# Kernel tuning notes

Hardware: AMD Instinct MI355X
Metric: run time of the kernel (lower is better)

The kernel has to match this reference:

```python
import jax, jax.numpy as jnp
import numpy as np

N_EMBD = 1024
N_HEAD = 16
B, T = 4, 2048
EPS = 1e-5


def setup_inputs() -> dict:
    key = jax.random.key(0)
    ks = jax.random.split(key, 12)
    s = 0.02
    d, dff = N_EMBD, 4 * N_EMBD
    return {
        "x": jax.random.normal(ks[0], (B, T, d), dtype=jnp.float32),
        "ln1_w": jnp.ones((d,), jnp.float32),
        "ln1_b": jnp.zeros((d,), jnp.float32),
        "ln2_w": jnp.ones((d,), jnp.float32),
        "ln2_b": jnp.zeros((d,), jnp.float32),
        "w_attn": jax.random.normal(ks[1], (d, 3 * d), jnp.float32) * s,
        "b_attn": jnp.zeros((3 * d,), jnp.float32),
        "w_proj": jax.random.normal(ks[2], (d, d), jnp.float32) * s,
        "b_proj": jnp.zeros((d,), jnp.float32),
        "w_fc": jax.random.normal(ks[3], (d, dff), jnp.float32) * s,
        "b_fc": jnp.zeros((dff,), jnp.float32),
        "w_fc2": jax.random.normal(ks[4], (dff, d), jnp.float32) * s,
        "b_fc2": jnp.zeros((d,), jnp.float32),
    }


def _layernorm(x, w, b):
    mu = jnp.mean(x, axis=-1, keepdims=True)
    var = jnp.mean(jnp.square(x - mu), axis=-1, keepdims=True)
    return (x - mu) * jax.lax.rsqrt(var + EPS) * w + b


def reference(x, ln1_w, ln1_b, ln2_w, ln2_b, w_attn, b_attn, w_proj, b_proj,
              w_fc, b_fc, w_fc2, b_fc2):
    Bx, Tx, C = x.shape
    hd = C // N_HEAD
    # --- attention branch ---
    h = _layernorm(x, ln1_w, ln1_b)
    qkv = h @ w_attn + b_attn  # [B,T,3C]
    q, k, v = jnp.split(qkv, 3, axis=-1)
    q = q.reshape(Bx, Tx, N_HEAD, hd).transpose(0, 2, 1, 3)  # [B,H,T,hd]
    k = k.reshape(Bx, Tx, N_HEAD, hd).transpose(0, 2, 1, 3)
    v = v.reshape(Bx, Tx, N_HEAD, hd).transpose(0, 2, 1, 3)
    att = jnp.einsum("bhqd,bhkd->bhqk", q, k) * (1.0 / np.sqrt(hd))
    causal = jnp.tril(jnp.ones((Tx, Tx), dtype=bool))
    att = jnp.where(causal[None, None], att, -jnp.inf)
    att = jax.nn.softmax(att, axis=-1)
    y = jnp.einsum("bhqk,bhkd->bhqd", att, v)
    y = y.transpose(0, 2, 1, 3).reshape(Bx, Tx, C)
    x = x + (y @ w_proj + b_proj)
    # --- mlp branch ---
    h2 = _layernorm(x, ln2_w, ln2_b)
    m = jax.nn.gelu(h2 @ w_fc + b_fc, approximate=False)
    x = x + (m @ w_fc2 + b_fc2)
    return x
```

## Files before the change

### kernel.cpp

```cpp
#include <hip/hip_runtime.h>
#include <hip/hip_bf16.h>
#include <math.h>

typedef __bf16 bf16;
typedef __bf16 bf16x4 __attribute__((ext_vector_type(4)));
typedef __bf16 bf16x8 __attribute__((ext_vector_type(8)));
typedef float f32x4 __attribute__((ext_vector_type(4)));

__device__ __forceinline__ void gload_lds16(const bf16* g, bf16* l) {
  __builtin_amdgcn_global_load_lds(
      (const __attribute__((address_space(1))) void*)g,
      (__attribute__((address_space(3))) void*)l, 16, 0, 0);
}

#define MF(a, b, c) __builtin_amdgcn_mfma_f32_16x16x32_bf16((a), (b), (c), 0, 0, 0)
#define VM4_BAR()  asm volatile("s_waitcnt vmcnt(4)\ns_barrier" ::: "memory")
#define VM2_BAR()  asm volatile("s_waitcnt vmcnt(2)\ns_barrier" ::: "memory")
#define VM0_BAR()  asm volatile("s_waitcnt vmcnt(0)\ns_barrier" ::: "memory")
#define LGK0_SB()  do { asm volatile("s_waitcnt lgkmcnt(0)" ::: "memory"); \
                        __builtin_amdgcn_sched_barrier(0); } while (0)

template <int EPI, int KSPLIT>
__global__ __launch_bounds__(512, 2)
void gemmq(const bf16* __restrict__ A, const bf16* __restrict__ BT,
           const float* __restrict__ bias, const float* __restrict__ res,
           void* __restrict__ Cout, void* __restrict__ Cout2,
           int M, int N, int K)
{
  __shared__ alignas(16) bf16 lsA[2][16384];
  __shared__ alignas(16) bf16 lsB[2][16384];

  int nbn = N >> 8;
  int nwg = (M >> 8) * nbn;
  int bid = blockIdx.x;
  int ks = 0;
  if (KSPLIT == 2) { ks = (bid >= nwg) ? 1 : 0; bid -= ks * nwg; }
  int cpx = nwg >> 3;
  int wg  = (bid & 7) * cpx + (bid >> 3);
  int m0 = (wg / nbn) << 8;
  int n0 = (wg % nbn) << 8;

  int t = threadIdx.x;
  int l = t & 63, w = t >> 6;
  int wr = (w >> 2) << 6;
  int wc = (w & 3) << 5;
  int lr = l & 15, lg = l >> 4;

  int kb0 = (KSPLIT == 2) ? ks * (K >> 1) : 0;
  int nt = (K / KSPLIT) >> 6;

  const bf16* Ag = A  + (size_t)m0 * K + kb0;
  const bf16* Bg = BT + (size_t)n0 * K + kb0;

  int swz0 = (lg ^ (lr & 7)) << 3;
  int swz1 = swz0 ^ 32;
  int aRow = (wr + lr) << 6;
  int bRow = (wc + lr) << 6;

  const bf16* srcA[2]; const bf16* srcB[2];
#pragma unroll
  for (int j = 0; j < 2; ++j) {
    int ci = j * 512 + t;
    int r = ci >> 3;
    int g = (ci & 7) ^ (r & 7);
    srcA[j] = Ag + (size_t)r * K + g * 8;
    srcB[j] = Bg + (size_t)r * K + g * 8;
  }
  size_t qA = (size_t)128 * K;

#define STAGE_A(q, kofs, db) do { \
  _Pragma("unroll") \
  for (int j = 0; j < 2; ++j) \
    gload_lds16(srcA[j] + (q) * qA + (kofs), &lsA[db][(q) * 8192 + (j * 512 + t) * 8]); \
} while (0)
#define STAGE_B(q, kofs, db) do { \
  _Pragma("unroll") \
  for (int j = 0; j < 2; ++j) \
    gload_lds16(srcB[j] + (q) * qA + (kofs), &lsB[db][(q) * 8192 + (j * 512 + t) * 8]); \
} while (0)

  f32x4 acc[2][2][4][2];
  f32x4 zero = {0.f, 0.f, 0.f, 0.f};
#pragma unroll
  for (int qa = 0; qa < 2; ++qa)
#pragma unroll
    for (int qb = 0; qb < 2; ++qb)
#pragma unroll
      for (int mi = 0; mi < 4; ++mi)
#pragma unroll
        for (int ni = 0; ni < 2; ++ni) acc[qa][qb][mi][ni] = zero;

  STAGE_A(0, 0, 0);
  STAGE_B(0, 0, 0);
  STAGE_B(1, 0, 0);
  STAGE_A(1, 0, 0);

  bf16x8 afr[4][2], bfr0[2][2], bfr1[2][2];

  for (int T = 0; T < nt; ++T) {
    int c = T & 1, d = c ^ 1;
    bool st = (T + 1 < nt);
    int k64 = (T + 1) << 6;
    const bf16* pa = &lsA[c][0];
    const bf16* pb = &lsB[c][0];

    VM4_BAR();
#pragma unroll
    for (int mi = 0; mi < 4; ++mi) {
      afr[mi][0] = *(const bf16x8*)(pa + aRow + mi * 1024 + swz0);
      afr[mi][1] = *(const bf16x8*)(pa + aRow + mi * 1024 + swz1);
    }
#pragma unroll
    for (int ni = 0; ni < 2; ++ni) {
      bfr0[ni][0] = *(const bf16x8*)(pb + bRow + ni * 1024 + swz0);
      bfr0[ni][1] = *(const bf16x8*)(pb + bRow + ni * 1024 + swz1);
    }
    if (st) STAGE_A(0, k64, d);
    LGK0_SB();
    __builtin_amdgcn_s_setprio(1);
#pragma unroll
    for (int mi = 0; mi < 4; ++mi)
#pragma unroll
      for (int ni = 0; ni < 2; ++ni)
#pragma unroll
        for (int kk = 0; kk < 2; ++kk)
          acc[0][0][mi][ni] = MF(afr[mi][kk], bfr0[ni][kk], acc[0][0][mi][ni]);
    __builtin_amdgcn_s_setprio(0);

    if (st) VM4_BAR(); else VM2_BAR();
#pragma unroll
    for (int ni = 0; ni < 2; ++ni) {
      bfr1[ni][0] = *(const bf16x8*)(pb + 8192 + bRow + ni * 1024 + swz0);
      bfr1[ni][1] = *(const bf16x8*)(pb + 8192 + bRow + ni * 1024 + swz1);
    }
    if (st) STAGE_B(0, k64, d);
    LGK0_SB();
    __builtin_amdgcn_s_setprio(1);
#pragma unroll
    for (int mi = 0; mi < 4; ++mi)
#pragma unroll
      for (int ni = 0; ni < 2; ++ni)
#pragma unroll
        for (int kk = 0; kk < 2; ++kk)
          acc[0][1][mi][ni] = MF(afr[mi][kk], bfr1[ni][kk], acc[0][1][mi][ni]);
    __builtin_amdgcn_s_setprio(0);

    if (st) VM4_BAR(); else VM0_BAR();
#pragma unroll
    for (int mi = 0; mi < 4; ++mi) {
      afr[mi][0] = *(const bf16x8*)(pa + 8192 + aRow + mi * 1024 + swz0);
      afr[mi][1] = *(const bf16x8*)(pa + 8192 + aRow + mi * 1024 + swz1);
    }
    if (st) STAGE_B(1, k64, d);
    LGK0_SB();
    __builtin_amdgcn_s_setprio(1);
#pragma unroll
    for (int mi = 0; mi < 4; ++mi)
#pragma unroll
      for (int ni = 0; ni < 2; ++ni)
#pragma unroll
        for (int kk = 0; kk < 2; ++kk)
          acc[1][1][mi][ni] = MF(afr[mi][kk], bfr1[ni][kk], acc[1][1][mi][ni]);
    __builtin_amdgcn_s_setprio(0);

    if (st) STAGE_A(1, k64, d);
    __builtin_amdgcn_s_setprio(1);
#pragma unroll
    for (int mi = 0; mi < 4; ++mi)
#pragma unroll
      for (int ni = 0; ni < 2; ++ni)
#pragma unroll
        for (int kk = 0; kk < 2; ++kk)
          acc[1][0][mi][ni] = MF(afr[mi][kk], bfr0[ni][kk], acc[1][0][mi][ni]);
    __builtin_amdgcn_s_setprio(0);
  }

  bf16* Pb = (bf16*)((KSPLIT == 2 && ks) ? Cout2 : Cout);
#pragma unroll
  for (int qa = 0; qa < 2; ++qa)
#pragma unroll
    for (int mi = 0; mi < 4; ++mi) {
      int row = m0 + qa * 128 + wr + mi * 16 + lg * 4;
#pragma unroll
      for (int qb = 0; qb < 2; ++qb)
#pragma unroll
        for (int ni = 0; ni < 2; ++ni) {
          int col = n0 + qb * 128 + wc + ni * 16 + lr;
          float bv = (EPI == 3) ? 0.f : bias[col];
          f32x4 a = acc[qa][qb][mi][ni];
#pragma unroll
          for (int r = 0; r < 4; ++r) {
            float v = a[r] + bv;
            size_t idx = (size_t)(row + r) * N + col;
            if (EPI == 0)      Pb[idx] = (bf16)v;
            else if (EPI == 1) ((float*)Cout)[idx] = v + res[idx];
            else if (EPI == 2) Pb[idx] = (bf16)(0.5f * v * (1.f + erff(v * 0.70710678118654752f)));
            else               Pb[idx] = (bf16)v;
          }
        }
    }
#undef STAGE_A
#undef STAGE_B
}

__global__ __launch_bounds__(256)
void combine2(const bf16* __restrict__ p0, const bf16* __restrict__ p1,
              const float* __restrict__ bias, const float* __restrict__ res,
              float* __restrict__ out)
{
  int i = (blockIdx.x * 256 + threadIdx.x) * 8;
  bf16x8 a = *(const bf16x8*)(p0 + i);
  bf16x8 b = *(const bf16x8*)(p1 + i);
  int c = i & 1023;
#pragma unroll
  for (int j = 0; j < 8; ++j)
    out[i + j] = (float)a[j] + (float)b[j] + bias[c + j] + res[i + j];
}

__global__ __launch_bounds__(256)
void combine_ln(const bf16* __restrict__ p0, const bf16* __restrict__ p1,
                const float* __restrict__ bias, const float* __restrict__ res,
                const float* __restrict__ lnw, const float* __restrict__ lnb,
                float* __restrict__ x1, bf16* __restrict__ hout)
{
  int row = blockIdx.x;
  int t = threadIdx.x;
  size_t i0 = (size_t)row * 1024 + t * 4;
  bf16x4 a = *(const bf16x4*)(p0 + i0);
  bf16x4 b = *(const bf16x4*)(p1 + i0);
  float4 r = *(const float4*)(res + i0);
  float4 bi = ((const float4*)bias)[t];
  float v0 = (float)a[0] + (float)b[0] + bi.x + r.x;
  float v1 = (float)a[1] + (float)b[1] + bi.y + r.y;
  float v2 = (float)a[2] + (float)b[2] + bi.z + r.z;
  float v3 = (float)a[3] + (float)b[3] + bi.w + r.w;
  float4 vv = {v0, v1, v2, v3};
  *(float4*)(x1 + i0) = vv;
  float s  = v0 + v1 + v2 + v3;
  float sq = v0 * v0 + v1 * v1 + v2 * v2 + v3 * v3;
#pragma unroll
  for (int off = 32; off >= 1; off >>= 1) {
    s  += __shfl_xor(s, off);
    sq += __shfl_xor(sq, off);
  }
  __shared__ float ps[4], pq[4];
  if ((t & 63) == 0) { ps[t >> 6] = s; pq[t >> 6] = sq; }
  __syncthreads();
  s  = ps[0] + ps[1] + ps[2] + ps[3];
  sq = pq[0] + pq[1] + pq[2] + pq[3];
  float mu  = s * (1.f / 1024.f);
  float var = sq * (1.f / 1024.f) - mu * mu;
  float rstd = rsqrtf(var + 1e-5f);
  float4 wv = ((const float4*)lnw)[t];
  float4 bv = ((const float4*)lnb)[t];
  hout[i0 + 0] = (bf16)((v0 - mu) * rstd * wv.x + bv.x);
  hout[i0 + 1] = (bf16)((v1 - mu) * rstd * wv.y + bv.y);
  hout[i0 + 2] = (bf16)((v2 - mu) * rstd * wv.z + bv.z);
  hout[i0 + 3] = (bf16)((v3 - mu) * rstd * wv.w + bv.w);
}

__global__ __launch_bounds__(256)
void ln_bf16(const float* __restrict__ x, const float* __restrict__ w,
             const float* __restrict__ b, bf16* __restrict__ out)
{
  int row = blockIdx.x;
  int t = threadIdx.x;
  float4 v = ((const float4*)(x + (size_t)row * 1024))[t];
  float s  = v.x + v.y + v.z + v.w;
  float sq = v.x * v.x + v.y * v.y + v.z * v.z + v.w * v.w;
#pragma unroll
  for (int off = 32; off >= 1; off >>= 1) {
    s  += __shfl_xor(s, off);
    sq += __shfl_xor(sq, off);
  }
  __shared__ float ps[4], pq[4];
  if ((t & 63) == 0) { ps[t >> 6] = s; pq[t >> 6] = sq; }
  __syncthreads();
  s  = ps[0] + ps[1] + ps[2] + ps[3];
  sq = pq[0] + pq[1] + pq[2] + pq[3];
  float mu  = s * (1.f / 1024.f);
  float var = sq * (1.f / 1024.f) - mu * mu;
  float rstd = rsqrtf(var + 1e-5f);
  float4 wv = ((const float4*)w)[t];
  float4 bv = ((const float4*)b)[t];
  size_t o0 = (size_t)row * 1024 + t * 4;
  out[o0 + 0] = (bf16)((v.x - mu) * rstd * wv.x + bv.x);
  out[o0 + 1] = (bf16)((v.y - mu) * rstd * wv.y + bv.y);
  out[o0 + 2] = (bf16)((v.z - mu) * rstd * wv.z + bv.z);
  out[o0 + 3] = (bf16)((v.w - mu) * rstd * wv.w + bv.w);
}

__global__ __launch_bounds__(256)
void transpose_cast(const float* __restrict__ W, bf16* __restrict__ WT, int K, int N)
{
  __shared__ float tile[32][33];
  int bk = blockIdx.x * 32, bn = blockIdx.y * 32;
  int tx = threadIdx.x & 31, ty = threadIdx.x >> 5;
#pragma unroll
  for (int i = ty; i < 32; i += 8)
    tile[i][tx] = W[(size_t)(bk + i) * N + bn + tx];
  __syncthreads();
#pragma unroll
  for (int i = ty; i < 32; i += 8)
    WT[(size_t)(bn + i) * K + bk + tx] = (bf16)tile[tx][i];
}

__global__ __launch_bounds__(256)
void vtrans(const bf16* __restrict__ qkv, bf16* __restrict__ vt)
{
  __shared__ alignas(16) bf16 tile[64 * 64];
  int bh = blockIdx.x;
  int b = bh >> 4, h = bh & 15;
  int t0 = blockIdx.y * 64;
  int t = threadIdx.x;
#pragma unroll
  for (int i = 0; i < 2; ++i) {
    int c = i * 256 + t;
    int tt = c >> 3, d8 = c & 7;
    bf16x8 v = *(const bf16x8*)(qkv + (size_t)(b * 2048 + t0 + tt) * 3072 + 2048 + h * 64 + d8 * 8);
    *(bf16x8*)&tile[(tt * 8 + (d8 ^ (tt >> 3))) * 8] = v;
  }
  __syncthreads();
#pragma unroll
  for (int i = 0; i < 2; ++i) {
    int c = i * 256 + t;
    int d = c >> 3, tt8 = c & 7;
    bf16x8 o;
#pragma unroll
    for (int j = 0; j < 8; ++j) {
      int row = tt8 * 8 + j;
      o[j] = tile[(row * 8 + ((d >> 3) ^ (row >> 3))) * 8 + (d & 7)];
    }
    *(bf16x8*)(vt + (size_t)(bh * 64 + d) * 2048 + t0 + tt8 * 8) = o;
  }
}

__global__ __launch_bounds__(256)
void attn_flash(const bf16* __restrict__ qkv, const bf16* __restrict__ vt,
                bf16* __restrict__ y)
{
  __shared__ alignas(16) bf16 lk[2][4096];
  __shared__ alignas(16) bf16 lv[2][4096];
  __shared__ alignas(16) bf16 lp[4][16 * 64];

  int bid = blockIdx.x;
  int bh = bid & 63;
  int qb = 31 - (bid >> 6);
  int b = bh >> 4, h = bh & 15;
  int t = threadIdx.x;
  int w = t >> 6, l = t & 63;
  int lr = l & 15, lg = l >> 4;
  int q0 = qb * 64;
  int qw = q0 + w * 16;
  const size_t RS = 3072;
  const float SCL = 0.18033688011112042f;

  const bf16* qbase = qkv + (size_t)(b * 2048) * RS + h * 64;
  const bf16* kbase = qkv + (size_t)(b * 2048) * RS + 1024 + h * 64;
  const bf16* vtb   = vt + (size_t)(bh * 64) * 2048;

  bf16x8 qf[2];
#pragma unroll
  for (int kk = 0; kk < 2; ++kk)
    qf[kk] = *(const bf16x8*)(qbase + (size_t)(qw + lr) * RS + kk * 32 + lg * 8);

  const bf16* pK[2]; const bf16* pV[2]; int dst[2];
#pragma unroll
  for (int i = 0; i < 2; ++i) {
    int c = i * 256 + t;
    int row = c >> 3, c8 = c & 7;
    int sc8 = c8 ^ (row & 7);
    pK[i] = kbase + (size_t)row * RS + sc8 * 8;
    pV[i] = vtb + (size_t)row * 2048 + sc8 * 8;
    dst[i] = c * 8;
  }

  f32x4 zero = {0.f, 0.f, 0.f, 0.f};
  f32x4 o[4];
#pragma unroll
  for (int ni = 0; ni < 4; ++ni) o[ni] = zero;
  float lo[4] = {0.f, 0.f, 0.f, 0.f};

  int nkb = qb + 1;
#pragma unroll
  for (int i = 0; i < 2; ++i) {
    gload_lds16(pK[i], &lk[0][dst[i]]);
    gload_lds16(pV[i], &lv[0][dst[i]]);
  }

  for (int kb = 0; kb < nkb; ++kb) {
    int cur = kb & 1;
    int k0 = kb * 64;
    VM0_BAR();
    if (kb + 1 < nkb) {
#pragma unroll
      for (int i = 0; i < 2; ++i) {
        pK[i] += 64 * RS;
        pV[i] += 64;
        gload_lds16(pK[i], &lk[cur ^ 1][dst[i]]);
        gload_lds16(pV[i], &lv[cur ^ 1][dst[i]]);
      }
    }

    f32x4 s[4];
#pragma unroll
    for (int j = 0; j < 4; ++j) s[j] = zero;
#pragma unroll
    for (int kk = 0; kk < 2; ++kk)
#pragma unroll
      for (int j = 0; j < 4; ++j) {
        int krow = j * 16 + lr;
        bf16x8 kf = *(const bf16x8*)&lk[cur][krow * 64 + (((4 * kk + lg) ^ (krow & 7)) * 8)];
        s[j] = MF(qf[kk], kf, s[j]);
      }

    bool needmask = (kb == qb);
    float p[4][4];
#pragma unroll
    for (int r = 0; r < 4; ++r) {
      int tq = qw + lg * 4 + r;
#pragma unroll
      for (int j = 0; j < 4; ++j) {
        float v = s[j][r] * SCL;
        if (needmask && (k0 + j * 16 + lr > tq)) v = -1e30f;
        p[j][r] = exp2f(v);
      }
      lo[r] += (p[0][r] + p[1][r]) + (p[2][r] + p[3][r]);
    }

#pragma unroll
    for (int r = 0; r < 4; ++r) {
      int qr = lg * 4 + r;
#pragma unroll
      for (int j = 0; j < 4; ++j) {
        int ch = (2 * j + (lr >> 3)) ^ (qr & 7);
        lp[w][qr * 64 + ch * 8 + (lr & 7)] = (bf16)p[j][r];
      }
    }
    bf16x8 pa[2];
#pragma unroll
    for (int kf = 0; kf < 2; ++kf)
      pa[kf] = *(const bf16x8*)&lp[w][lr * 64 + (((4 * kf + lg) ^ (lr & 7)) * 8)];

#pragma unroll
    for (int ni = 0; ni < 4; ++ni)
#pragma unroll
      for (int kf = 0; kf < 2; ++kf) {
        int d = ni * 16 + lr;
        bf16x8 vf = *(const bf16x8*)&lv[cur][d * 64 + (((4 * kf + lg) ^ (d & 7)) * 8)];
        o[ni] = MF(pa[kf], vf, o[ni]);
      }
  }

#pragma unroll
  for (int r = 0; r < 4; ++r) {
#pragma unroll
    for (int off = 1; off < 16; off <<= 1) lo[r] += __shfl_xor(lo[r], off);
    lo[r] = 1.f / lo[r];
  }
#pragma unroll
  for (int ni = 0; ni < 4; ++ni)
#pragma unroll
    for (int r = 0; r < 4; ++r) {
      int tq = qw + lg * 4 + r;
      y[(size_t)(b * 2048 + tq) * 1024 + h * 64 + ni * 16 + lr] = (bf16)(o[ni][r] * lo[r]);
    }
}

extern "C" void kernel_launch(void* const* d_in, const int* in_sizes, int n_in,
                              void* d_out, int out_size, void* d_ws, size_t ws_size,
                              hipStream_t stream) {
  (void)in_sizes; (void)n_in; (void)out_size; (void)ws_size;
  const float* x      = (const float*)d_in[0];
  const float* ln1w   = (const float*)d_in[1];
  const float* ln1b   = (const float*)d_in[2];
  const float* ln2w   = (const float*)d_in[3];
  const float* ln2b   = (const float*)d_in[4];
  const float* w_attn = (const float*)d_in[5];
  const float* b_attn = (const float*)d_in[6];
  const float* w_proj = (const float*)d_in[7];
  const float* b_proj = (const float*)d_in[8];
  const float* w_fc   = (const float*)d_in[9];
  const float* b_fc   = (const float*)d_in[10];
  const float* w_fc2  = (const float*)d_in[11];
  const float* b_fc2  = (const float*)d_in[12];
  float* out = (float*)d_out;

  char* p = (char*)d_ws;
  bf16*  h     = (bf16*)p;  p += (size_t)8192 * 1024 * 2;
  bf16*  qkv   = (bf16*)p;
  bf16*  mbuf  = (bf16*)p;  p += (size_t)8192 * 3072 * 2;
  bf16*  ybuf  = (bf16*)p;  p += (size_t)8192 * 1024 * 2;
  float* x1    = (float*)p; p += (size_t)8192 * 1024 * 4;
  bf16*  wqkvT = (bf16*)p;  p += (size_t)3072 * 1024 * 2;
  bf16*  wprojT= (bf16*)p;  p += (size_t)1024 * 1024 * 2;
  bf16*  wfcT  = (bf16*)p;  p += (size_t)4096 * 1024 * 2;
  bf16*  wfc2T = (bf16*)p;  p += (size_t)1024 * 4096 * 2;
  bf16*  vt    = (bf16*)x1;
  bf16*  pp0   = qkv;
  bf16*  pp1   = qkv + (size_t)8192 * 1024;
  bf16*  sp0   = h;
  bf16*  sp1   = wqkvT;

  transpose_cast<<<dim3(1024 / 32, 3072 / 32), 256, 0, stream>>>(w_attn, wqkvT, 1024, 3072);
  transpose_cast<<<dim3(1024 / 32, 1024 / 32), 256, 0, stream>>>(w_proj, wprojT, 1024, 1024);
  transpose_cast<<<dim3(1024 / 32, 4096 / 32), 256, 0, stream>>>(w_fc,   wfcT,  1024, 4096);
  transpose_cast<<<dim3(4096 / 32, 1024 / 32), 256, 0, stream>>>(w_fc2,  wfc2T, 4096, 1024);

  ln_bf16<<<8192, 256, 0, stream>>>(x, ln1w, ln1b, h);
  gemmq<0, 1><<<384, 512, 0, stream>>>(h, wqkvT, b_attn, nullptr, qkv, nullptr, 8192, 3072, 1024);
  vtrans<<<dim3(64, 32), 256, 0, stream>>>(qkv, vt);
  attn_flash<<<2048, 256, 0, stream>>>(qkv, vt, ybuf);
  gemmq<3, 2><<<256, 512, 0, stream>>>(ybuf, wprojT, nullptr, nullptr, pp0, pp1, 8192, 1024, 1024);
  combine_ln<<<8192, 256, 0, stream>>>(pp0, pp1, b_proj, x, ln2w, ln2b, x1, h);
  gemmq<2, 1><<<512, 512, 0, stream>>>(h, wfcT, b_fc, nullptr, mbuf, nullptr, 8192, 4096, 1024);
  gemmq<3, 2><<<256, 512, 0, stream>>>(mbuf, wfc2T, nullptr, nullptr, sp0, sp1, 8192, 1024, 4096);
  combine2<<<4096, 256, 0, stream>>>(sp0, sp1, b_fc2, x1, out);
}
```

Measured before the change: 409.5 us.

## Replace interleaved quarter-tile staging with single wait and bulk prefetch per K-step

The GEMM main loop used to interleave four quarter-tile global-to-LDS stages with fine-grained vmcnt waits and barriers between four MFMA groups. It now waits for all loads (vmcnt 0) once per K-step, issues all next-tile stages together, then reads every A/B fragment from LDS and runs all four MFMA groups back to back. This simplifies synchronization and cuts the number of barriers, but it raises register pressure with more live fragments and loses the overlap of load completion with partial compute. Dropping the explicit lgkmcnt wait leaves fragment ordering to the compiler.

```diff
diff --git a/kernel.cpp b/kernel.cpp
--- a/kernel.cpp
+++ b/kernel.cpp
@@ -14,11 +14,7 @@
 }
 
 #define MF(a, b, c) __builtin_amdgcn_mfma_f32_16x16x32_bf16((a), (b), (c), 0, 0, 0)
-#define VM4_BAR()  asm volatile("s_waitcnt vmcnt(4)\ns_barrier" ::: "memory")
-#define VM2_BAR()  asm volatile("s_waitcnt vmcnt(2)\ns_barrier" ::: "memory")
 #define VM0_BAR()  asm volatile("s_waitcnt vmcnt(0)\ns_barrier" ::: "memory")
-#define LGK0_SB()  do { asm volatile("s_waitcnt lgkmcnt(0)" ::: "memory"); \
-                        __builtin_amdgcn_sched_barrier(0); } while (0)
 
 template <int EPI, int KSPLIT>
 __global__ __launch_bounds__(512, 2)
@@ -95,7 +91,7 @@
   STAGE_B(1, 0, 0);
   STAGE_A(1, 0, 0);
 
-  bf16x8 afr[4][2], bfr0[2][2], bfr1[2][2];
+  bf16x8 a0[4][2], a1[4][2], b0[2][2], b1[2][2];
 
   for (int T = 0; T < nt; ++T) {
     int c = T & 1, d = c ^ 1;
@@ -104,19 +100,35 @@
     const bf16* pa = &lsA[c][0];
     const bf16* pb = &lsB[c][0];
 
-    VM4_BAR();
+    VM0_BAR();
+    if (st) {
+      STAGE_A(0, k64, d);
+      STAGE_B(0, k64, d);
+      STAGE_B(1, k64, d);
+      STAGE_A(1, k64, d);
+    }
+
 #pragma unroll
     for (int mi = 0; mi < 4; ++mi) {
-      afr[mi][0] = *(const bf16x8*)(pa + aRow + mi * 1024 + swz0);
-      afr[mi][1] = *(const bf16x8*)(pa + aRow + mi * 1024 + swz1);
+      a0[mi][0] = *(const bf16x8*)(pa + aRow + mi * 1024 + swz0);
+      a0[mi][1] = *(const bf16x8*)(pa + aRow + mi * 1024 + swz1);
     }
 #pragma unroll
     for (int ni = 0; ni < 2; ++ni) {
-      bfr0[ni][0] = *(const bf16x8*)(pb + bRow + ni * 1024 + swz0);
-      bfr0[ni][1] = *(const bf16x8*)(pb + bRow + ni * 1024 + swz1);
-    }
-    if (st) STAGE_A(0, k64, d);
-    LGK0_SB();
+      b0[ni][0] = *(const bf16x8*)(pb + bRow + ni * 1024 + swz0);
+      b0[ni][1] = *(const bf16x8*)(pb + bRow + ni * 1024 + swz1);
+    }
+#pragma unroll
+    for (int ni = 0; ni < 2; ++ni) {
+      b1[ni][0] = *(const bf16x8*)(pb + 8192 + bRow + ni * 1024 + swz0);
+      b1[ni][1] = *(const bf16x8*)(pb + 8192 + bRow + ni * 1024 + swz1);
+    }
+#pragma unroll
+    for (int mi = 0; mi < 4; ++mi) {
+      a1[mi][0] = *(const bf16x8*)(pa + 8192 + aRow + mi * 1024 + swz0);
+      a1[mi][1] = *(const bf16x8*)(pa + 8192 + aRow + mi * 1024 + swz1);
+    }
+
     __builtin_amdgcn_s_setprio(1);
 #pragma unroll
     for (int mi = 0; mi < 4; ++mi)
@@ -124,54 +136,28 @@
       for (int ni = 0; ni < 2; ++ni)
 #pragma unroll
         for (int kk = 0; kk < 2; ++kk)
-          acc[0][0][mi][ni] = MF(afr[mi][kk], bfr0[ni][kk], acc[0][0][mi][ni]);
-    __builtin_amdgcn_s_setprio(0);
-
-    if (st) VM4_BAR(); else VM2_BAR();
-#pragma unroll
-    for (int ni = 0; ni < 2; ++ni) {
-      bfr1[ni][0] = *(const bf16x8*)(pb + 8192 + bRow + ni * 1024 + swz0);
-      bfr1[ni][1] = *(const bf16x8*)(pb + 8192 + bRow + ni * 1024 + swz1);
-    }
-    if (st) STAGE_B(0, k64, d);
-    LGK0_SB();
-    __builtin_amdgcn_s_setprio(1);
+          acc[0][0][mi][ni] = MF(a0[mi][kk], b0[ni][kk], acc[0][0][mi][ni]);
 #pragma unroll
     for (int mi = 0; mi < 4; ++mi)
 #pragma unroll
       for (int ni = 0; ni < 2; ++ni)
 #pragma unroll
         for (int kk = 0; kk < 2; ++kk)
-          acc[0][1][mi][ni] = MF(afr[mi][kk], bfr1[ni][kk], acc[0][1][mi][ni]);
-    __builtin_amdgcn_s_setprio(0);
-
-    if (st) VM4_BAR(); else VM0_BAR();
-#pragma unroll
-    for (int mi = 0; mi < 4; ++mi) {
-      afr[mi][0] = *(const bf16x8*)(pa + 8192 + aRow + mi * 1024 + swz0);
-      afr[mi][1] = *(const bf16x8*)(pa + 8192 + aRow + mi * 1024 + swz1);
-    }
-    if (st) STAGE_B(1, k64, d);
-    LGK0_SB();
-    __builtin_amdgcn_s_setprio(1);
+          acc[0][1][mi][ni] = MF(a0[mi][kk], b1[ni][kk], acc[0][1][mi][ni]);
 #pragma unroll
     for (int mi = 0; mi < 4; ++mi)
 #pragma unroll
       for (int ni = 0; ni < 2; ++ni)
 #pragma unroll
         for (int kk = 0; kk < 2; ++kk)
-          acc[1][1][mi][ni] = MF(afr[mi][kk], bfr1[ni][kk], acc[1][1][mi][ni]);
-    __builtin_amdgcn_s_setprio(0);
-
-    if (st) STAGE_A(1, k64, d);
-    __builtin_amdgcn_s_setprio(1);
+          acc[1][1][mi][ni] = MF(a1[mi][kk], b1[ni][kk], acc[1][1][mi][ni]);
 #pragma unroll
     for (int mi = 0; mi < 4; ++mi)
 #pragma unroll
       for (int ni = 0; ni < 2; ++ni)
 #pragma unroll
         for (int kk = 0; kk < 2; ++kk)
-          acc[1][0][mi][ni] = MF(afr[mi][kk], bfr0[ni][kk], acc[1][0][mi][ni]);
+          acc[1][0][mi][ni] = MF(a1[mi][kk], b0[ni][kk], acc[1][0][mi][ni]);
     __builtin_amdgcn_s_setprio(0);
   }
 
```

After: 422.2 us. 3.1% more time.

## Double attention query tile to 128 rows and fold softmax scale into QKV epilogue

Applied to the files above, without the earlier changes.

The flash attention kernel now runs 8 waves per block over 128 query rows instead of 4 waves over 64. Each K/V tile loaded into LDS is therefore shared by twice as many query rows, which halves global K/V traffic and block count. The causal mask check becomes per-wave, since blocks now span two diagonal key tiles. The softmax scale (with log2e) is moved into the QKV GEMM epilogue for the Q columns, removing a multiply per score. This rounds scaled Q to bf16, which slightly changes numerics, and the larger blocks may reduce occupancy and leave diagonal-tile waves with more masked work.

```diff
diff --git a/kernel.cpp b/kernel.cpp
--- a/kernel.cpp
+++ b/kernel.cpp
@@ -175,6 +175,7 @@
     __builtin_amdgcn_s_setprio(0);
   }
 
+  const float SCLQ = 0.18033688011112042f;
   bf16* Pb = (bf16*)((KSPLIT == 2 && ks) ? Cout2 : Cout);
 #pragma unroll
   for (int qa = 0; qa < 2; ++qa)
@@ -195,6 +196,7 @@
             if (EPI == 0)      Pb[idx] = (bf16)v;
             else if (EPI == 1) ((float*)Cout)[idx] = v + res[idx];
             else if (EPI == 2) Pb[idx] = (bf16)(0.5f * v * (1.f + erff(v * 0.70710678118654752f)));
+            else if (EPI == 4) Pb[idx] = (bf16)((col < 1024) ? v * SCLQ : v);
             else               Pb[idx] = (bf16)v;
           }
         }
@@ -335,25 +337,24 @@
   }
 }
 
-__global__ __launch_bounds__(256)
+__global__ __launch_bounds__(512)
 void attn_flash(const bf16* __restrict__ qkv, const bf16* __restrict__ vt,
                 bf16* __restrict__ y)
 {
   __shared__ alignas(16) bf16 lk[2][4096];
   __shared__ alignas(16) bf16 lv[2][4096];
-  __shared__ alignas(16) bf16 lp[4][16 * 64];
+  __shared__ alignas(16) bf16 lp[8][16 * 64];
 
   int bid = blockIdx.x;
   int bh = bid & 63;
-  int qb = 31 - (bid >> 6);
+  int qb = 15 - (bid >> 6);
   int b = bh >> 4, h = bh & 15;
   int t = threadIdx.x;
   int w = t >> 6, l = t & 63;
   int lr = l & 15, lg = l >> 4;
-  int q0 = qb * 64;
+  int q0 = qb * 128;
   int qw = q0 + w * 16;
   const size_t RS = 3072;
-  const float SCL = 0.18033688011112042f;
 
   const bf16* qbase = qkv + (size_t)(b * 2048) * RS + h * 64;
   const bf16* kbase = qkv + (size_t)(b * 2048) * RS + 1024 + h * 64;
@@ -364,16 +365,11 @@
   for (int kk = 0; kk < 2; ++kk)
     qf[kk] = *(const bf16x8*)(qbase + (size_t)(qw + lr) * RS + kk * 32 + lg * 8);
 
-  const bf16* pK[2]; const bf16* pV[2]; int dst[2];
-#pragma unroll
-  for (int i = 0; i < 2; ++i) {
-    int c = i * 256 + t;
-    int row = c >> 3, c8 = c & 7;
-    int sc8 = c8 ^ (row & 7);
-    pK[i] = kbase + (size_t)row * RS + sc8 * 8;
-    pV[i] = vtb + (size_t)row * 2048 + sc8 * 8;
-    dst[i] = c * 8;
-  }
+  int row = t >> 3, c8 = t & 7;
+  int sc8 = c8 ^ (row & 7);
+  const bf16* pK = kbase + (size_t)row * RS + sc8 * 8;
+  const bf16* pV = vtb + (size_t)row * 2048 + sc8 * 8;
+  int dst = t * 8;
 
   f32x4 zero = {0.f, 0.f, 0.f, 0.f};
   f32x4 o[4];
@@ -381,25 +377,19 @@
   for (int ni = 0; ni < 4; ++ni) o[ni] = zero;
   float lo[4] = {0.f, 0.f, 0.f, 0.f};
 
-  int nkb = qb + 1;
-#pragma unroll
-  for (int i = 0; i < 2; ++i) {
-    gload_lds16(pK[i], &lk[0][dst[i]]);
-    gload_lds16(pV[i], &lv[0][dst[i]]);
-  }
+  int nkb = 2 * qb + 2;
+  gload_lds16(pK, &lk[0][dst]);
+  gload_lds16(pV, &lv[0][dst]);
 
   for (int kb = 0; kb < nkb; ++kb) {
     int cur = kb & 1;
     int k0 = kb * 64;
     VM0_BAR();
     if (kb + 1 < nkb) {
-#pragma unroll
-      for (int i = 0; i < 2; ++i) {
-        pK[i] += 64 * RS;
-        pV[i] += 64;
-        gload_lds16(pK[i], &lk[cur ^ 1][dst[i]]);
-        gload_lds16(pV[i], &lv[cur ^ 1][dst[i]]);
-      }
+      pK += 64 * RS;
+      pV += 64;
+      gload_lds16(pK, &lk[cur ^ 1][dst]);
+      gload_lds16(pV, &lv[cur ^ 1][dst]);
     }
 
     f32x4 s[4];
@@ -414,14 +404,14 @@
         s[j] = MF(qf[kk], kf, s[j]);
       }
 
-    bool needmask = (kb == qb);
+    bool needmask = (k0 + 63 > qw);
     float p[4][4];
 #pragma unroll
     for (int r = 0; r < 4; ++r) {
       int tq = qw + lg * 4 + r;
 #pragma unroll
       for (int j = 0; j < 4; ++j) {
-        float v = s[j][r] * SCL;
+        float v = s[j][r];
         if (needmask && (k0 + j * 16 + lr > tq)) v = -1e30f;
         p[j][r] = exp2f(v);
       }
@@ -508,9 +498,9 @@
   transpose_cast<<<dim3(4096 / 32, 1024 / 32), 256, 0, stream>>>(w_fc2,  wfc2T, 4096, 1024);
 
   ln_bf16<<<8192, 256, 0, stream>>>(x, ln1w, ln1b, h);
-  gemmq<0, 1><<<384, 512, 0, stream>>>(h, wqkvT, b_attn, nullptr, qkv, nullptr, 8192, 3072, 1024);
+  gemmq<4, 1><<<384, 512, 0, stream>>>(h, wqkvT, b_attn, nullptr, qkv, nullptr, 8192, 3072, 1024);
   vtrans<<<dim3(64, 32), 256, 0, stream>>>(qkv, vt);
-  attn_flash<<<2048, 256, 0, stream>>>(qkv, vt, ybuf);
+  attn_flash<<<1024, 512, 0, stream>>>(qkv, vt, ybuf);
   gemmq<3, 2><<<256, 512, 0, stream>>>(ybuf, wprojT, nullptr, nullptr, pp0, pp1, 8192, 1024, 1024);
   combine_ln<<<8192, 256, 0, stream>>>(pp0, pp1, b_proj, x, ln2w, ln2b, x1, h);
   gemmq<2, 1><<<512, 512, 0, stream>>>(h, wfcT, b_fc, nullptr, mbuf, nullptr, 8192, 4096, 1024);
```

Result: no change. 410.9 us (+0.3%).
